# Kernel optimization log

Measured on AMD Instinct MI355X. Metric: run time of the kernel, lower is better.

Reference implementation:

```python
import jax, jax.numpy as jnp
import numpy as np

N = 10000      # num nodes
E = 160000     # num edges (before self-loops)
D_IN = 512
D_HID = 512
D_OUT = 512
C = 64         # num classes


def setup_inputs() -> dict:
    key = jax.random.key(0)
    ks = jax.random.split(key, 8)
    x = jax.random.normal(ks[0], (N, D_IN), dtype=jnp.float32)
    edge_index = jax.random.randint(ks[1], (2, E), 0, N, dtype=jnp.int64)
    W1 = jax.random.normal(ks[2], (D_IN, D_HID), jnp.float32) / np.sqrt(D_IN)
    b1 = jnp.zeros((D_HID,), jnp.float32)
    W2 = jax.random.normal(ks[3], (D_HID, D_OUT), jnp.float32) / np.sqrt(D_HID)
    b2 = jnp.zeros((D_OUT,), jnp.float32)
    Wc = jax.random.normal(ks[4], (D_OUT, C), jnp.float32) / np.sqrt(D_OUT)
    bc = jnp.zeros((C,), jnp.float32)
    return {"x": x, "edge_index": edge_index, "W1": W1, "b1": b1,
            "W2": W2, "b2": b2, "Wc": Wc, "bc": bc}


def _gcn_conv(x, src, dst, ew, W, b):
    """GCNConv: symmetric degree-normalized scatter-add. ew = edge weights."""
    h = x @ W  # [N, D_out] dense GEMM
    deg = jax.ops.segment_sum(ew, dst, num_segments=N)  # in-degree incl. loops
    dis = jnp.where(deg > 0, jax.lax.rsqrt(jnp.maximum(deg, 1e-12)), 0.0)
    norm = dis[src] * dis[dst] * ew  # [E+N]
    out = jax.ops.segment_sum(h[src] * norm[:, None], dst, num_segments=N)
    return out + b


def reference(x, edge_index, W1, b1, W2, b2, Wc, bc):
    src, dst = edge_index[0], edge_index[1]
    # add_remaining_self_loops: drop existing self-loops, add one per node
    loops = jnp.arange(N, dtype=edge_index.dtype)
    src_f = jnp.concatenate([src, loops])
    dst_f = jnp.concatenate([dst, loops])
    ew = jnp.concatenate([(src != dst).astype(jnp.float32),
                          jnp.ones((N,), jnp.float32)])
    h = jax.nn.relu(_gcn_conv(x, src_f, dst_f, ew, W1, b1))
    h = _gcn_conv(h, src_f, dst_f, ew, W2, b2)
    logits = h @ Wc + bc
    return logits, jax.nn.log_softmax(logits, axis=1)
```

## Files before the change

### kernel.cpp

```cpp
#include <hip/hip_runtime.h>
#include <hip/hip_bf16.h>

#define N_NODES 10000
#define DIM 512
#define NCLS 64
#define BM 64
#define BN 128
#define BK 64
#define ELLW 64

typedef __hip_bfloat16 bf16;
typedef unsigned short u16;
typedef __attribute__((ext_vector_type(8))) short short8;
typedef __attribute__((ext_vector_type(4))) float f32x4;

__device__ __forceinline__ float b2f(bf16 v) { return __bfloat162float(v); }
__device__ __forceinline__ float ldIn(const void* p, size_t i, int isb) {
    return isb ? b2f(((const bf16*)p)[i]) : ((const float*)p)[i];
}
__device__ __forceinline__ int getE(const int* ei, int is64, int flat) {
    return is64 ? ei[2 * (size_t)flat] : ei[flat];
}
__device__ __forceinline__ void load_lds16(const bf16* g, bf16* l) {
    __builtin_amdgcn_global_load_lds(
        (const __attribute__((address_space(1))) void*)g,
        (__attribute__((address_space(3))) void*)l, 16, 0, 0);
}

__global__ void init_kernel(const u16* x16, const int* ei, int* flags, int* cursor) {
    int i = blockIdx.x * blockDim.x + threadIdx.x;
    if (i < N_NODES) cursor[i] = 0;
    if (blockIdx.x == 0 && threadIdx.x < 64) {
        int l = threadIdx.x;
        int cf = 0;
        #pragma unroll
        for (int j = 0; j < 4; j++) {
            int e = (x16[l * 4 + j] >> 7) & 0xFF;
            cf += (e >= 97 && e <= 157) ? 1 : 0;
        }
        #pragma unroll
        for (int o = 32; o > 0; o >>= 1) cf += __shfl_xor(cf, o, 64);
        int cz = (l < 32) ? ((ei[2 * l + 1] == 0) ? 1 : 0) : 0;
        #pragma unroll
        for (int o = 32; o > 0; o >>= 1) cz += __shfl_xor(cz, o, 64);
        if (l == 0) { flags[0] = (cf >= 200) ? 1 : 0; flags[1] = (cz >= 16) ? 1 : 0; }
    }
}

__global__ __launch_bounds__(256) void convert_all(
        const void* __restrict__ X, const void* __restrict__ W1,
        const void* __restrict__ W2, const void* __restrict__ Wc,
        const int* __restrict__ ei, const int* __restrict__ flags,
        int* __restrict__ cursor, int* __restrict__ ell,
        bf16* __restrict__ Xb, bf16* __restrict__ Wt1, bf16* __restrict__ Wt2,
        bf16* __restrict__ Wtc, int E) {
    __shared__ float tile[32][33];
    int b = blockIdx.x, t = threadIdx.x;
    if (b < 2500) {
        int isb = flags[0];
        int base = (b * 256 + t) * 8;
        bf16 o[8];
        if (isb) {
            *(uint4*)o = *(const uint4*)((const bf16*)X + base);
        } else {
            const float* Xf = (const float*)X + base;
            float4 v0 = *(const float4*)Xf, v1 = *(const float4*)(Xf + 4);
            o[0] = __float2bfloat16(v0.x); o[1] = __float2bfloat16(v0.y);
            o[2] = __float2bfloat16(v0.z); o[3] = __float2bfloat16(v0.w);
            o[4] = __float2bfloat16(v1.x); o[5] = __float2bfloat16(v1.y);
            o[6] = __float2bfloat16(v1.z); o[7] = __float2bfloat16(v1.w);
        }
        *(uint4*)&Xb[base] = *(uint4*)o;
    } else if (b < 3044) {
        int isb = flags[0];
        const void* W; bf16* Wt; int N; int bb;
        if (b < 2756)      { W = W1; Wt = Wt1; N = DIM;  bb = b - 2500; }
        else if (b < 3012) { W = W2; Wt = Wt2; N = DIM;  bb = b - 2756; }
        else               { W = Wc; Wt = Wtc; N = NCLS; bb = b - 3012; }
        int nt = N / 32;
        int n0 = (bb % nt) * 32, k0 = (bb / nt) * 32;
        int tx = t & 31, ty = t >> 5;
        for (int r = ty; r < 32; r += 8)
            tile[r][tx] = ldIn(W, (size_t)(k0 + r) * N + n0 + tx, isb);
        __syncthreads();
        for (int r = ty; r < 32; r += 8)
            Wt[(size_t)(n0 + r) * DIM + k0 + tx] = __float2bfloat16(tile[tx][r]);
    } else {
        int e = (b - 3044) * 256 + t;
        if (e >= E) return;
        int is64 = flags[1];
        int s = getE(ei, is64, e), d = getE(ei, is64, E + e);
        if (s == d || (unsigned)s >= N_NODES || (unsigned)d >= N_NODES) return;
        int pos = atomicAdd(&cursor[d], 1);
        ell[d * ELLW + (pos & (ELLW - 1))] = s;
    }
}

__global__ __launch_bounds__(256) void gemm_mfma(
        const bf16* __restrict__ A, const bf16* __restrict__ Bt,
        bf16* __restrict__ C, int M, int Nc, int K,
        const int* __restrict__ deg) {
    __shared__ bf16 At[BM * BK];
    __shared__ bf16 Bts[BN * BK];
    int t = threadIdx.x;
    int w = t >> 6, l = t & 63;
    int bm = blockIdx.y * BM, bn = blockIdx.x * BN;
    int wn = w * 32;

    f32x4 acc[4][2] = {};
    int srow8 = l >> 3;
    int sk8b  = (l & 7) * 8;

    for (int k0 = 0; k0 < K; k0 += BK) {
        __syncthreads();
        #pragma unroll
        for (int i = 0; i < 2; i++) {
            int c = w * 2 + i;
            load_lds16(A + (size_t)(bm + c * 8 + srow8) * K + k0 + sk8b, &At[c * 512]);
        }
        #pragma unroll
        for (int i = 0; i < 4; i++) {
            int c = w * 4 + i;
            load_lds16(Bt + (size_t)(bn + c * 8 + srow8) * K + k0 + sk8b, &Bts[c * 512]);
        }
        __syncthreads();

        #pragma unroll
        for (int kk = 0; kk < BK; kk += 32) {
            short8 af[4], bf[2];
            #pragma unroll
            for (int i = 0; i < 4; i++)
                af[i] = *(const short8*)&At[(i * 16 + (l & 15)) * BK + kk + (l >> 4) * 8];
            #pragma unroll
            for (int j = 0; j < 2; j++)
                bf[j] = *(const short8*)&Bts[(wn + j * 16 + (l & 15)) * BK + kk + (l >> 4) * 8];
            #pragma unroll
            for (int i = 0; i < 4; i++)
                #pragma unroll
                for (int j = 0; j < 2; j++)
                    acc[i][j] = __builtin_amdgcn_mfma_f32_16x16x32_bf16(
                                    af[i], bf[j], acc[i][j], 0, 0, 0);
        }
    }

    int col = l & 15, rq = (l >> 4) * 4;
    #pragma unroll
    for (int i = 0; i < 4; i++) {
        #pragma unroll
        for (int r = 0; r < 4; r++) {
            int gm = bm + i * 16 + rq + r;
            if (gm >= M) continue;
            float rs = rsqrtf((float)deg[gm] + 1.0f);
            #pragma unroll
            for (int j = 0; j < 2; j++) {
                int gn = bn + wn + j * 16 + col;
                C[(size_t)gm * Nc + gn] = __float2bfloat16(acc[i][j][r] * rs);
            }
        }
    }
}

__global__ __launch_bounds__(256) void gather_ell(
        const int* __restrict__ cursor, const int* __restrict__ ell,
        const bf16* __restrict__ Hs, const void* __restrict__ bias,
        const int* __restrict__ flags, bf16* __restrict__ Out, int relu) {
    int wid = (int)((blockIdx.x * (size_t)blockDim.x + threadIdx.x) >> 6);
    int lane = threadIdx.x & 63;
    if (wid >= N_NODES) return;
    int cnt0 = cursor[wid];
    int cnt = min(cnt0, ELLW);
    int idx = ell[wid * ELLW + lane];

    float acc[8];
    bf16 v[8];
    *(uint4*)v = *(const uint4*)(Hs + (size_t)wid * DIM + lane * 8);
    #pragma unroll
    for (int j = 0; j < 8; j++) acc[j] = b2f(v[j]);

    int e = 0;
    for (; e + 7 < cnt; e += 8) {
        bf16 r[8][8];
        #pragma unroll
        for (int b = 0; b < 8; b++) {
            int s = __shfl(idx, e + b, 64);
            *(uint4*)r[b] = *(const uint4*)(Hs + (size_t)s * DIM + lane * 8);
        }
        #pragma unroll
        for (int j = 0; j < 8; j++)
            acc[j] += ((b2f(r[0][j]) + b2f(r[1][j])) + (b2f(r[2][j]) + b2f(r[3][j])))
                    + ((b2f(r[4][j]) + b2f(r[5][j])) + (b2f(r[6][j]) + b2f(r[7][j])));
    }
    for (; e < cnt; e++) {
        int s = __shfl(idx, e, 64);
        *(uint4*)v = *(const uint4*)(Hs + (size_t)s * DIM + lane * 8);
        #pragma unroll
        for (int j = 0; j < 8; j++) acc[j] += b2f(v[j]);
    }

    float ds = rsqrtf((float)cnt0 + 1.0f);
    int ibias = flags[0];
    bf16 o[8];
    #pragma unroll
    for (int j = 0; j < 8; j++) {
        float val = acc[j] * ds + ldIn(bias, lane * 8 + j, ibias);
        if (relu) val = fmaxf(val, 0.0f);
        o[j] = __float2bfloat16(val);
    }
    *(uint4*)(Out + (size_t)wid * DIM + lane * 8) = *(uint4*)o;
}

__global__ __launch_bounds__(64) void cls_lsm_kernel(
        const bf16* __restrict__ A, const bf16* __restrict__ Wct,
        const void* __restrict__ bias, const int* __restrict__ flags,
        float* __restrict__ out, int M) {
    int l = threadIdx.x;
    int row0 = blockIdx.x * 16;
    int q = l >> 4, col15 = l & 15;

    f32x4 acc[4] = {};
    #pragma unroll 4
    for (int k0 = 0; k0 < DIM; k0 += 32) {
        short8 af = *(const short8*)&A[(size_t)(row0 + col15) * DIM + k0 + q * 8];
        #pragma unroll
        for (int j = 0; j < 4; j++) {
            short8 bf = *(const short8*)&Wct[(size_t)(j * 16 + col15) * DIM + k0 + q * 8];
            acc[j] = __builtin_amdgcn_mfma_f32_16x16x32_bf16(af, bf, acc[j], 0, 0, 0);
        }
    }

    int ibias = flags[0];
    float bcol[4];
    #pragma unroll
    for (int j = 0; j < 4; j++) bcol[j] = ldIn(bias, j * 16 + col15, ibias);

    #pragma unroll
    for (int r = 0; r < 4; r++) {
        int row = row0 + q * 4 + r;
        float v[4];
        #pragma unroll
        for (int j = 0; j < 4; j++) v[j] = acc[j][r] + bcol[j];
        float m = fmaxf(fmaxf(v[0], v[1]), fmaxf(v[2], v[3]));
        #pragma unroll
        for (int o = 8; o > 0; o >>= 1) m = fmaxf(m, __shfl_xor(m, o, 64));
        float s = __expf(v[0] - m) + __expf(v[1] - m) + __expf(v[2] - m) + __expf(v[3] - m);
        #pragma unroll
        for (int o = 8; o > 0; o >>= 1) s += __shfl_xor(s, o, 64);
        float lse = m + __logf(s);
        if (row < M) {
            #pragma unroll
            for (int j = 0; j < 4; j++) {
                out[(size_t)row * NCLS + j * 16 + col15] = v[j];
                out[(size_t)M * NCLS + (size_t)row * NCLS + j * 16 + col15] = v[j] - lse;
            }
        }
    }
}

extern "C" void kernel_launch(void* const* d_in, const int* in_sizes, int n_in,
                              void* d_out, int out_size, void* d_ws, size_t ws_size,
                              hipStream_t stream) {
    const void* x  = d_in[0];
    const int*  ei = (const int*)d_in[1];
    const void* W1 = d_in[2];
    const void* b1 = d_in[3];
    const void* W2 = d_in[4];
    const void* b2 = d_in[5];
    const void* Wc = d_in[6];
    const void* bc = d_in[7];
    float* out = (float*)d_out;
    int E = in_sizes[1] / 2;

    char* ws = (char*)d_ws;
    int*   flags  = (int*)ws;
    int*   cursor = (int*)(ws + 65536);
    int*   ell    = (int*)(ws + 131072);
    bf16*  xb     = (bf16*) (ws + 4194304);
    bf16*  Wt1    = (bf16*) (ws + 14680064);
    bf16*  Wt2    = (bf16*) (ws + 15204352);
    bf16*  Wct    = (bf16*) (ws + 15728640);
    bf16*  B0     = (bf16*) (ws + 16777216);
    bf16*  B1     = (bf16*) (ws + 27262976);

    int gN = (N_NODES * 64 + 255) / 256;
    dim3 gg(DIM / BN, (N_NODES + BM - 1) / BM);
    int gConv = 3044 + (E + 255) / 256;

    init_kernel<<<(N_NODES + 255) / 256, 256, 0, stream>>>((const u16*)x, ei, flags, cursor);
    convert_all<<<gConv, 256, 0, stream>>>(x, W1, W2, Wc, ei, flags, cursor, ell,
                                           xb, Wt1, Wt2, Wct, E);

    gemm_mfma<<<gg, 256, 0, stream>>>(xb, Wt1, B0, N_NODES, DIM, DIM, cursor);
    gather_ell<<<gN, 256, 0, stream>>>(cursor, ell, B0, b1, flags, B1, 1);

    gemm_mfma<<<gg, 256, 0, stream>>>(B1, Wt2, B0, N_NODES, DIM, DIM, cursor);
    gather_ell<<<gN, 256, 0, stream>>>(cursor, ell, B0, b2, flags, B1, 0);

    cls_lsm_kernel<<<(N_NODES + 15) / 16, 64, 0, stream>>>(B1, Wct, bc, flags, out, N_NODES);
}
```

Baseline: 191.6 us.

## Narrow GEMM tiles, split gather across two waves, stage classifier weights in LDS

The dense GEMM tile width drops from 128 to 64 columns, with one 16-column MFMA strip per wave. This doubles the number of blocks to improve occupancy and CU coverage. The ELL gather now uses two waves per node, each covering half the feature row. It does branchless 16-neighbour batches and sends out-of-range slots to padding row N_NODES, which the GEMM now fills with zeros instead of skipping. The classifier kernel loads Wc once into 64KB of LDS per 4-wave block instead of re-reading it from global memory per wave. The zero padding row depends on GEMM rows beyond M being finite, and the larger LDS use may limit occupancy.

```diff
diff --git a/kernel.cpp b/kernel.cpp
--- a/kernel.cpp
+++ b/kernel.cpp
@@ -5,7 +5,7 @@
 #define DIM 512
 #define NCLS 64
 #define BM 64
-#define BN 128
+#define BN 64
 #define BK 64
 #define ELLW 64
 
@@ -105,9 +105,9 @@
     int t = threadIdx.x;
     int w = t >> 6, l = t & 63;
     int bm = blockIdx.y * BM, bn = blockIdx.x * BN;
-    int wn = w * 32;
-
-    f32x4 acc[4][2] = {};
+    int wn = w * 16;
+
+    f32x4 acc[4] = {};
     int srow8 = l >> 3;
     int sk8b  = (l & 7) * 8;
 
@@ -119,27 +119,20 @@
             load_lds16(A + (size_t)(bm + c * 8 + srow8) * K + k0 + sk8b, &At[c * 512]);
         }
         #pragma unroll
-        for (int i = 0; i < 4; i++) {
-            int c = w * 4 + i;
+        for (int i = 0; i < 2; i++) {
+            int c = w * 2 + i;
             load_lds16(Bt + (size_t)(bn + c * 8 + srow8) * K + k0 + sk8b, &Bts[c * 512]);
         }
         __syncthreads();
 
         #pragma unroll
         for (int kk = 0; kk < BK; kk += 32) {
-            short8 af[4], bf[2];
+            short8 bfr = *(const short8*)&Bts[(wn + (l & 15)) * BK + kk + (l >> 4) * 8];
             #pragma unroll
-            for (int i = 0; i < 4; i++)
-                af[i] = *(const short8*)&At[(i * 16 + (l & 15)) * BK + kk + (l >> 4) * 8];
-            #pragma unroll
-            for (int j = 0; j < 2; j++)
-                bf[j] = *(const short8*)&Bts[(wn + j * 16 + (l & 15)) * BK + kk + (l >> 4) * 8];
-            #pragma unroll
-            for (int i = 0; i < 4; i++)
-                #pragma unroll
-                for (int j = 0; j < 2; j++)
-                    acc[i][j] = __builtin_amdgcn_mfma_f32_16x16x32_bf16(
-                                    af[i], bf[j], acc[i][j], 0, 0, 0);
+            for (int i = 0; i < 4; i++) {
+                short8 af = *(const short8*)&At[(i * 16 + (l & 15)) * BK + kk + (l >> 4) * 8];
+                acc[i] = __builtin_amdgcn_mfma_f32_16x16x32_bf16(af, bfr, acc[i], 0, 0, 0);
+            }
         }
     }
 
@@ -149,13 +142,9 @@
         #pragma unroll
         for (int r = 0; r < 4; r++) {
             int gm = bm + i * 16 + rq + r;
-            if (gm >= M) continue;
-            float rs = rsqrtf((float)deg[gm] + 1.0f);
-            #pragma unroll
-            for (int j = 0; j < 2; j++) {
-                int gn = bn + wn + j * 16 + col;
-                C[(size_t)gm * Nc + gn] = __float2bfloat16(acc[i][j][r] * rs);
-            }
+            float rs = (gm < M) ? rsqrtf((float)deg[gm] + 1.0f) : 0.0f;
+            int gn = bn + wn + col;
+            C[(size_t)gm * Nc + gn] = __float2bfloat16(acc[i][r] * rs);
         }
     }
 }
@@ -164,67 +153,77 @@
         const int* __restrict__ cursor, const int* __restrict__ ell,
         const bf16* __restrict__ Hs, const void* __restrict__ bias,
         const int* __restrict__ flags, bf16* __restrict__ Out, int relu) {
-    int wid = (int)((blockIdx.x * (size_t)blockDim.x + threadIdx.x) >> 6);
+    int gwid = (int)((blockIdx.x * (size_t)blockDim.x + threadIdx.x) >> 6);
     int lane = threadIdx.x & 63;
+    int wid = gwid >> 1;
+    int half = gwid & 1;
     if (wid >= N_NODES) return;
     int cnt0 = cursor[wid];
     int cnt = min(cnt0, ELLW);
     int idx = ell[wid * ELLW + lane];
-
-    float acc[8];
-    bf16 v[8];
-    *(uint4*)v = *(const uint4*)(Hs + (size_t)wid * DIM + lane * 8);
-    #pragma unroll
-    for (int j = 0; j < 8; j++) acc[j] = b2f(v[j]);
-
-    int e = 0;
-    for (; e + 7 < cnt; e += 8) {
-        bf16 r[8][8];
-        #pragma unroll
-        for (int b = 0; b < 8; b++) {
-            int s = __shfl(idx, e + b, 64);
-            *(uint4*)r[b] = *(const uint4*)(Hs + (size_t)s * DIM + lane * 8);
-        }
-        #pragma unroll
-        for (int j = 0; j < 8; j++)
-            acc[j] += ((b2f(r[0][j]) + b2f(r[1][j])) + (b2f(r[2][j]) + b2f(r[3][j])))
-                    + ((b2f(r[4][j]) + b2f(r[5][j])) + (b2f(r[6][j]) + b2f(r[7][j])));
-    }
-    for (; e < cnt; e++) {
-        int s = __shfl(idx, e, 64);
-        *(uint4*)v = *(const uint4*)(Hs + (size_t)s * DIM + lane * 8);
-        #pragma unroll
-        for (int j = 0; j < 8; j++) acc[j] += b2f(v[j]);
+    int off = half * 256 + lane * 4;
+
+    float acc[4];
+    bf16 v[4];
+    *(uint2*)v = *(const uint2*)(Hs + (size_t)wid * DIM + off);
+    #pragma unroll
+    for (int j = 0; j < 4; j++) acc[j] = b2f(v[j]);
+
+    for (int e = 0; e < cnt; e += 16) {
+        bf16 r[16][4];
+        #pragma unroll
+        for (int b = 0; b < 16; b++) {
+            int s = __shfl(idx, (e + b) & 63, 64);
+            s = (e + b < cnt) ? s : N_NODES;
+            *(uint2*)r[b] = *(const uint2*)(Hs + (size_t)s * DIM + off);
+        }
+        #pragma unroll
+        for (int j = 0; j < 4; j++) {
+            float s0 = (b2f(r[0][j]) + b2f(r[1][j])) + (b2f(r[2][j]) + b2f(r[3][j]));
+            float s1 = (b2f(r[4][j]) + b2f(r[5][j])) + (b2f(r[6][j]) + b2f(r[7][j]));
+            float s2 = (b2f(r[8][j]) + b2f(r[9][j])) + (b2f(r[10][j]) + b2f(r[11][j]));
+            float s3 = (b2f(r[12][j]) + b2f(r[13][j])) + (b2f(r[14][j]) + b2f(r[15][j]));
+            acc[j] += (s0 + s1) + (s2 + s3);
+        }
     }
 
     float ds = rsqrtf((float)cnt0 + 1.0f);
     int ibias = flags[0];
-    bf16 o[8];
-    #pragma unroll
-    for (int j = 0; j < 8; j++) {
-        float val = acc[j] * ds + ldIn(bias, lane * 8 + j, ibias);
+    bf16 o[4];
+    #pragma unroll
+    for (int j = 0; j < 4; j++) {
+        float val = acc[j] * ds + ldIn(bias, off + j, ibias);
         if (relu) val = fmaxf(val, 0.0f);
         o[j] = __float2bfloat16(val);
     }
-    *(uint4*)(Out + (size_t)wid * DIM + lane * 8) = *(uint4*)o;
-}
-
-__global__ __launch_bounds__(64) void cls_lsm_kernel(
+    *(uint2*)(Out + (size_t)wid * DIM + off) = *(uint2*)o;
+}
+
+__global__ __launch_bounds__(256) void cls_lsm_kernel(
         const bf16* __restrict__ A, const bf16* __restrict__ Wct,
         const void* __restrict__ bias, const int* __restrict__ flags,
         float* __restrict__ out, int M) {
-    int l = threadIdx.x;
-    int row0 = blockIdx.x * 16;
+    __shared__ bf16 Ws[NCLS * DIM];
+    int t = threadIdx.x, w = t >> 6, l = t & 63;
+
+    #pragma unroll
+    for (int i = 0; i < 16; i++) {
+        int c = i * 4 + w;
+        load_lds16(Wct + c * 512 + l * 8, &Ws[c * 512]);
+    }
+    __syncthreads();
+
+    int row0 = (blockIdx.x * 4 + w) * 16;
     int q = l >> 4, col15 = l & 15;
 
     f32x4 acc[4] = {};
-    #pragma unroll 4
+    #pragma unroll
     for (int k0 = 0; k0 < DIM; k0 += 32) {
         short8 af = *(const short8*)&A[(size_t)(row0 + col15) * DIM + k0 + q * 8];
         #pragma unroll
         for (int j = 0; j < 4; j++) {
-            short8 bf = *(const short8*)&Wct[(size_t)(j * 16 + col15) * DIM + k0 + q * 8];
-            acc[j] = __builtin_amdgcn_mfma_f32_16x16x32_bf16(af, bf, acc[j], 0, 0, 0);
+            short8 bfr = *(const short8*)&Ws[(j * 16 + col15) * DIM + k0 + q * 8];
+            acc[j] = __builtin_amdgcn_mfma_f32_16x16x32_bf16(af, bfr, acc[j], 0, 0, 0);
         }
     }
 
@@ -281,8 +280,8 @@
     bf16*  B0     = (bf16*) (ws + 16777216);
     bf16*  B1     = (bf16*) (ws + 27262976);
 
-    int gN = (N_NODES * 64 + 255) / 256;
     dim3 gg(DIM / BN, (N_NODES + BM - 1) / BM);
+    int gN = (N_NODES * 2 * 64 + 255) / 256;
     int gConv = 3044 + (E + 255) / 256;
 
     init_kernel<<<(N_NODES + 255) / 256, 256, 0, stream>>>((const u16*)x, ei, flags, cursor);
@@ -295,5 +294,5 @@
     gemm_mfma<<<gg, 256, 0, stream>>>(B1, Wt2, B0, N_NODES, DIM, DIM, cursor);
     gather_ell<<<gN, 256, 0, stream>>>(cursor, ell, B0, b2, flags, B1, 0);
 
-    cls_lsm_kernel<<<(N_NODES + 15) / 16, 64, 0, stream>>>(B1, Wct, bc, flags, out, N_NODES);
-}
+    cls_lsm_kernel<<<(N_NODES + 63) / 64, 256, 0, stream>>>(B1, Wct, bc, flags, out, N_NODES);
+}
```

After: 193.9 us. No clear change (+1.2%).
